# Kernel tuning notes

Hardware: AMD Instinct MI355X
Metric: run time of the kernel (lower is better)

Reference implementation:

```python
import jax, jax.numpy as jnp
import numpy as np
from jax import lax

K = 3          # kernel size
PAD = 1        # (K-1)//2
C = 64         # channels
RED = 16       # channel-attention reduction


def conv2d(x, w, b=None):
    # x [B,C,H,W], w [O,I,kh,kw]
    out = lax.conv_general_dilated(x, w, (1, 1), 'SAME',
                                   dimension_numbers=('NCHW', 'OIHW', 'NCHW'))
    if b is not None:
        out = out + b[None, :, None, None]
    return out


def rcab(x, w1, b1, w2, b2, caw1, cab1, caw2, cab2):
    res = conv2d(x, w1, b1)
    res = jax.nn.relu(res)
    res = conv2d(res, w2, b2)
    # channel attention: global avg pool -> 1x1 conv -> relu -> 1x1 conv -> sigmoid
    y = jnp.mean(res, axis=(2, 3), keepdims=True)
    y = jax.nn.relu(conv2d(y, caw1, cab1))
    y = jax.nn.sigmoid(conv2d(y, caw2, cab2))
    return res * y + x


def deform_conv(x, inter, fea, off_w, off_b, mask_w, mask_b, weight):
    # Modulated deformable conv: offsets/mask predicted from concat(inter, fea).
    B, Cc, H, W = x.shape
    KK = K * K
    guide = jnp.concatenate([inter, fea], axis=1)
    offset = conv2d(guide, off_w, off_b)                    # [B, 2*KK, H, W]
    mask = 2.0 * jax.nn.sigmoid(conv2d(guide, mask_w, mask_b))  # [B, KK, H, W]
    off = offset.reshape(B, KK, 2, H, W)
    oy, ox = off[:, :, 0], off[:, :, 1]                     # [B, KK, H, W]

    ky = (jnp.arange(KK) // K - PAD).astype(x.dtype)        # kernel tap y offsets
    kx = (jnp.arange(KK) % K - PAD).astype(x.dtype)
    ii = jnp.arange(H, dtype=x.dtype)[None, None, :, None]
    jj = jnp.arange(W, dtype=x.dtype)[None, None, None, :]
    ys = ii + ky[None, :, None, None] + oy                  # [B, KK, H, W]
    xs = jj + kx[None, :, None, None] + ox

    y0 = jnp.floor(ys); x0 = jnp.floor(xs)
    wy1 = ys - y0; wy0 = 1.0 - wy1
    wx1 = xs - x0; wx0 = 1.0 - wx1
    y0i = y0.astype(jnp.int32); x0i = x0.astype(jnp.int32)
    y1i = y0i + 1; x1i = x0i + 1

    x_flat = x.reshape(B, Cc, H * W)

    def gather(yi, xi):
        valid = ((yi >= 0) & (yi < H) & (xi >= 0) & (xi < W)).astype(x.dtype)
        idx = jnp.clip(yi, 0, H - 1) * W + jnp.clip(xi, 0, W - 1)   # [B,KK,H,W]
        idx = idx.reshape(B, KK * H * W)
        g = jax.vmap(lambda f, i: jnp.take(f, i, axis=1))(x_flat, idx)
        return g.reshape(B, Cc, KK, H, W) * valid[:, None]

    val = (gather(y0i, x0i) * (wy0 * wx0)[:, None]
           + gather(y0i, x1i) * (wy0 * wx1)[:, None]
           + gather(y1i, x0i) * (wy1 * wx0)[:, None]
           + gather(y1i, x1i) * (wy1 * wx1)[:, None])     # [B,C,KK,H,W]
    val = val * mask[:, None]
    w_flat = weight.reshape(weight.shape[0], Cc, KK)        # [O,I,KK]
    return jnp.einsum('bckhw,ock->bohw', val, w_flat)


def setup_inputs() -> dict:
    key = jax.random.key(0)
    ks = jax.random.split(key, 20)
    B, H, W = 4, 192, 192
    f32 = jnp.float32
    d = {
        'x':     jax.random.normal(ks[0], (B, C, H, W), f32),
        'inter': jax.random.normal(ks[1], (B, C, H, W), f32),
        'fea':   jax.random.normal(ks[2], (B, C, H, W), f32),
        # RCAB
        'rcab_w1': jax.random.normal(ks[3], (C, C, 3, 3), f32) * 0.05,
        'rcab_b1': jnp.zeros((C,), f32),
        'rcab_w2': jax.random.normal(ks[4], (C, C, 3, 3), f32) * 0.05,
        'rcab_b2': jnp.zeros((C,), f32),
        'ca_w1': jax.random.normal(ks[5], (C // RED, C, 1, 1), f32) * 0.05,
        'ca_b1': jnp.zeros((C // RED,), f32),
        'ca_w2': jax.random.normal(ks[6], (C, C // RED, 1, 1), f32) * 0.05,
        'ca_b2': jnp.zeros((C,), f32),
        # deformable conv offset/mask branch (input = concat(inter, fea) -> 2C)
        'off_w': jax.random.normal(ks[7], (2 * K * K, 2 * C, 3, 3), f32) * 0.01,
        'off_b': jnp.zeros((2 * K * K,), f32),
        'mask_w': jax.random.normal(ks[8], (K * K, 2 * C, 3, 3), f32) * 0.01,
        'mask_b': jnp.zeros((K * K,), f32),
        'deform_w': jax.random.normal(ks[9], (C, C, K, K), f32) * 0.05,
        # final conv
        'conv_w': jax.random.normal(ks[10], (C, C, 3, 3), f32) * 0.05,
        'conv_b': jnp.zeros((C,), f32),
    }
    return d


def reference(x, inter, fea, rcab_w1, rcab_b1, rcab_w2, rcab_b2,
              ca_w1, ca_b1, ca_w2, ca_b2,
              off_w, off_b, mask_w, mask_b, deform_w, conv_w, conv_b):
    out1 = rcab(x, rcab_w1, rcab_b1, rcab_w2, rcab_b2, ca_w1, ca_b1, ca_w2, ca_b2)
    out2 = deform_conv(out1, inter, fea, off_w, off_b, mask_w, mask_b, deform_w)
    return conv2d(out2 + out1, conv_w, conv_b)
```

## Files before the change

kernel.cpp:

```cpp
#include <hip/hip_runtime.h>
#include <hip/hip_bf16.h>
#include <hip/hip_fp16.h>
#include <math.h>

#define HSZ 192
#define WSZ 192
#define HWSZ (192*192)
#define PH 194
#define PP (PH*PH)
#define NB 4

typedef __attribute__((ext_vector_type(8))) short short8;
typedef __attribute__((ext_vector_type(4))) float f32x4;

__device__ inline unsigned short f2bf(float f) { __hip_bfloat16 h = __float2bfloat16(f); return *(unsigned short*)&h; }
__device__ inline float bf2f(__hip_bfloat16 h) { return __bfloat162float(h); }
__device__ inline float bflo(unsigned u) { return __uint_as_float(u << 16); }
__device__ inline float bfhi(unsigned u) { return __uint_as_float(u & 0xffff0000u); }

#define GLDS(SRC, DST) __builtin_amdgcn_global_load_lds( \
    (const __attribute__((address_space(1))) unsigned int*)(const void*)(SRC), \
    (__attribute__((address_space(3))) unsigned int*)(void*)(DST), 16, 0, 0)

#define MFMA(A,B,C) __builtin_amdgcn_mfma_f32_16x16x32_bf16((A),(B),(C),0,0,0)

__global__ void zb2_k(__hip_bfloat16* xn, __hip_bfloat16* r1, __hip_bfloat16* out1,
                      __hip_bfloat16* cat) {
  int job = blockIdx.y;
  __hip_bfloat16* buf = job == 0 ? xn : job == 1 ? r1 : job == 2 ? out1 : cat;
  int Cn = (job == 3) ? 128 : 64;
  int cg8 = Cn >> 3;
  int tot = NB * 772 * cg8;
  int idx = blockIdx.x * 256 + threadIdx.x;
  if (idx >= tot) return;
  int cg = idx % cg8; int rem = idx / cg8;
  int e = rem % 772; int b = rem / 772;
  int h, w2;
  if (e < 194) { h = 0; w2 = e; }
  else if (e < 388) { h = 193; w2 = e - 194; }
  else if (e < 580) { h = e - 388 + 1; w2 = 0; }
  else { h = e - 580 + 1; w2 = 193; }
  uint4 z = make_uint4(0, 0, 0, 0);
  *(uint4*)&buf[(((size_t)b * PH + h) * PH + w2) * Cn + cg * 8] = z;
}

__global__ void wts_k(const float* __restrict__ rw1, const float* __restrict__ rw2,
                      const float* __restrict__ cw, const float* __restrict__ offw,
                      const float* __restrict__ maskw, const float* __restrict__ offb,
                      const float* __restrict__ maskb, const float* __restrict__ dwv,
                      short* wt1, short* wt2c, short* wtf, short* wtom, float* ob,
                      short* wtb, float* meanz) {
  int job = blockIdx.y;
  int idx = blockIdx.x * 256 + threadIdx.x;
  if (job < 3) {
    const float* src = job == 0 ? rw1 : job == 1 ? rw2 : cw;
    short* dst = job == 0 ? wt1 : job == 1 ? wt2c : wtf;
    int kk = idx >> 12, rem = idx & 4095;
    int co = rem >> 6, ci = rem & 63;
    dst[idx] = (short)f2bf(src[(co * 64 + ci) * 9 + kk]);
  } else if (job == 3) {
    int kk = idx >> 12, rem = idx & 4095;
    int co = rem >> 7, ci = rem & 127;
    float v = 0.f;
    if (co < 18) v = offw[(co * 128 + ci) * 9 + kk];
    else if (co < 27) v = maskw[((co - 18) * 128 + ci) * 9 + kk];
    wtom[idx] = (short)f2bf(v);
    if (idx < 32) ob[idx] = idx < 18 ? offb[idx] : (idx < 27 ? maskb[idx - 18] : 0.f);
  } else {
    int o = idx / 576, rem = idx - o * 576;
    int kk = rem >> 6, ci = rem & 63;
    wtb[idx] = (short)f2bf(dwv[(o * 64 + ci) * 9 + kk]);
    if (blockIdx.x == 0 && threadIdx.x < 256) meanz[threadIdx.x] = 0.f;
  }
}

__global__ __launch_bounds__(256) void cvt_k(const float* __restrict__ x,
    const float* __restrict__ inter, const float* __restrict__ fea,
    __hip_bfloat16* __restrict__ xn, __hip_bfloat16* __restrict__ cat) {
  int job = blockIdx.z;
  const float* src = job == 0 ? x : job == 1 ? inter : fea;
  __hip_bfloat16* dst = job == 0 ? xn : cat;
  int Cdst = job == 0 ? 64 : 128;
  int coff = job == 2 ? 64 : 0;
  __shared__ float s[64][65];
  int p0 = blockIdx.x * 64; int b = blockIdx.y;
  int lane = threadIdx.x & 63, g = threadIdx.x >> 6;
#pragma unroll
  for (int i = 0; i < 16; ++i) {
    int c = i * 4 + g;
    s[c][lane] = src[((size_t)b * 64 + c) * HWSZ + p0 + lane];
  }
  __syncthreads();
  int pix = threadIdx.x >> 2, cg = threadIdx.x & 3;
  int h = p0 / WSZ, w0 = p0 - h * WSZ + pix;
  size_t addr = (((size_t)b * PH + h + 1) * PH + 1 + w0) * Cdst + coff + cg * 16;
  unsigned pk2[8];
#pragma unroll
  for (int t = 0; t < 8; ++t)
    pk2[t] = (unsigned)f2bf(s[cg * 16 + 2 * t][pix]) | ((unsigned)f2bf(s[cg * 16 + 2 * t + 1][pix]) << 16);
  *(uint4*)&dst[addr]     = make_uint4(pk2[0], pk2[1], pk2[2], pk2[3]);
  *(uint4*)&dst[addr + 8] = make_uint4(pk2[4], pk2[5], pk2[6], pk2[7]);
}

template<int OUT_MODE, bool RELU, bool MEANACC>
__global__ __launch_bounds__(256, 2) void conv_mfma_k(
    const __hip_bfloat16* __restrict__ inp, const short* __restrict__ wt,
    const float* __restrict__ bias, __hip_bfloat16* __restrict__ outB,
    float* __restrict__ outF, float* __restrict__ meanout) {
  int flat = (blockIdx.x & 7) * 96 + (blockIdx.x >> 3);
  const int b = flat / 192, h = flat - (flat / 192) * 192;
  const int tid = threadIdx.x, lane = tid & 63, wid = tid >> 6;
  const int q = lane >> 4, r16 = lane & 15;
  __shared__ __align__(16) short tile[3 * 200 * 64];
  __shared__ float smean[4][64];

  {
    const char* gb = (const char*)(inp + ((size_t)b * PH + h) * (PH * 64));
    for (int s = wid; s < 75; s += 4) {
      int rr = s / 25, si = s - rr * 25;
      int pix = 8 * si + (lane >> 3);
      const char* src = gb + (size_t)rr * (PH * 128) + pix * 128
                      + ((((lane & 7) ^ ((lane >> 3) & 7))) << 4);
      GLDS(src, tile + rr * 12800 + si * 512);
    }
  }

  f32x4 acc[3][4];
  if (OUT_MODE == 0) {
#pragma unroll
    for (int nf = 0; nf < 4; ++nf) {
      float4 bv = *(const float4*)&bias[nf * 16 + q * 4];
      f32x4 v; v[0] = bv.x; v[1] = bv.y; v[2] = bv.z; v[3] = bv.w;
      acc[0][nf] = v; acc[1][nf] = v; acc[2][nf] = v;
    }
  } else {
#pragma unroll
    for (int nf = 0; nf < 4; ++nf) {
      float bs = bias[nf * 16 + r16];
      f32x4 v; v[0] = bs; v[1] = bs; v[2] = bs; v[3] = bs;
      acc[0][nf] = v; acc[1][nf] = v; acc[2][nf] = v;
    }
  }
  __syncthreads();

  const int wm0 = wid * 48;
  for (int kk = 0; kk < 9; ++kk) {
    const int ky = kk / 3, kx = kk - ky * 3;
    short8 bfr[2][4];
    const short* wk = wt + kk * 4096 + r16 * 64 + q * 8;
#pragma unroll
    for (int nf = 0; nf < 4; ++nf) {
      bfr[0][nf] = *(const short8*)(wk + nf * 1024);
      bfr[1][nf] = *(const short8*)(wk + nf * 1024 + 32);
    }
#pragma unroll
    for (int mf = 0; mf < 3; ++mf) {
      int pix = wm0 + mf * 16 + r16 + kx;
      const char* ab = (const char*)tile + ky * 25600 + pix * 128;
      int sw = (pix & 7) << 4;
      short8 a0 = *(const short8*)(ab + ((q << 4) ^ sw));
      short8 a1 = *(const short8*)(ab + (((q + 4) << 4) ^ sw));
#pragma unroll
      for (int nf = 0; nf < 4; ++nf) {
        if (OUT_MODE == 0) {
          acc[mf][nf] = MFMA(bfr[0][nf], a0, acc[mf][nf]);
          acc[mf][nf] = MFMA(bfr[1][nf], a1, acc[mf][nf]);
        } else {
          acc[mf][nf] = MFMA(a0, bfr[0][nf], acc[mf][nf]);
          acc[mf][nf] = MFMA(a1, bfr[1][nf], acc[mf][nf]);
        }
      }
    }
  }

  if (MEANACC) {
    float t[4][4];
#pragma unroll
    for (int nf = 0; nf < 4; ++nf)
#pragma unroll
      for (int rg = 0; rg < 4; ++rg)
        t[nf][rg] = acc[0][nf][rg] + acc[1][nf][rg] + acc[2][nf][rg];
#pragma unroll
    for (int m = 1; m < 16; m <<= 1)
#pragma unroll
      for (int nf = 0; nf < 4; ++nf)
#pragma unroll
        for (int rg = 0; rg < 4; ++rg)
          t[nf][rg] += __shfl_xor(t[nf][rg], m);
    if (r16 == 0)
#pragma unroll
      for (int nf = 0; nf < 4; ++nf)
#pragma unroll
        for (int rg = 0; rg < 4; ++rg)
          smean[wid][nf * 16 + q * 4 + rg] = t[nf][rg];
    __syncthreads();
    if (tid < 64)
      atomicAdd(&meanout[b * 64 + tid],
                (smean[0][tid] + smean[1][tid] + smean[2][tid] + smean[3][tid]) * (1.f / 36864.f));
  }

  if (OUT_MODE == 0) {
    __syncthreads();
#pragma unroll
    for (int mf = 0; mf < 3; ++mf)
#pragma unroll
      for (int nf = 0; nf < 4; ++nf) {
        f32x4 v = acc[mf][nf];
        if (RELU) { v[0] = fmaxf(v[0], 0.f); v[1] = fmaxf(v[1], 0.f); v[2] = fmaxf(v[2], 0.f); v[3] = fmaxf(v[3], 0.f); }
        unsigned lo = (unsigned)f2bf(v[0]) | ((unsigned)f2bf(v[1]) << 16);
        unsigned hi = (unsigned)f2bf(v[2]) | ((unsigned)f2bf(v[3]) << 16);
        int pix = wm0 + mf * 16 + r16;
        int byteoff = (pix * 128 + nf * 32 + q * 8) ^ ((pix & 7) << 4);
        *(uint2*)((char*)tile + byteoff) = make_uint2(lo, hi);
      }
    __syncthreads();
    char* orow = (char*)outB + ((((size_t)b * PH + h + 1) * PH + 1) * 64) * 2;
    for (int s = wid; s < 24; s += 4) {
      int pix = 8 * s + (lane >> 3);
      int g16 = ((lane & 7) ^ (pix & 7)) << 4;
      uint4 d = *(const uint4*)((const char*)tile + pix * 128 + g16);
      *(uint4*)(orow + pix * 128 + ((lane & 7) << 4)) = d;
    }
  } else {
    float* ob2 = outF + (size_t)b * 64 * HWSZ + h * WSZ;
#pragma unroll
    for (int mf = 0; mf < 3; ++mf)
#pragma unroll
      for (int nf = 0; nf < 4; ++nf) {
        int pix0 = wm0 + mf * 16 + q * 4;
        int co = nf * 16 + r16;
        *(f32x4*)&ob2[(size_t)co * HWSZ + pix0] = acc[mf][nf];
      }
  }
}

__global__ __launch_bounds__(256, 3) void offmask_mfma_k(
    const __hip_bfloat16* __restrict__ cat, const short* __restrict__ wt2,
    const float* __restrict__ ob, float* __restrict__ om) {
  const int h = blockIdx.x, b = blockIdx.y;
  const int tid = threadIdx.x, lane = tid & 63, wid = tid >> 6;
  const int q = lane >> 4, r16 = lane & 15;
  __shared__ __align__(16) short tile[200 * 128];

  f32x4 acc[3][2];
#pragma unroll
  for (int nf = 0; nf < 2; ++nf) {
    float bs = ob[nf * 16 + r16];
    f32x4 v; v[0] = bs; v[1] = bs; v[2] = bs; v[3] = bs;
    acc[0][nf] = v; acc[1][nf] = v; acc[2][nf] = v;
  }
  const char* gb = (const char*)(cat + ((size_t)b * PH + h) * (PH * 128));
  const int wm0 = wid * 48;

  for (int r = 0; r < 3; ++r) {
    __syncthreads();
    for (int s = wid; s < 50; s += 4) {
      int pix = 4 * s + (lane >> 4);
      const char* src = gb + (size_t)r * (PH * 256) + pix * 256
                      + ((((lane & 15) ^ (pix & 15))) << 4);
      GLDS(src, tile + s * 512);
    }
    __syncthreads();
    for (int kx = 0; kx < 3; ++kx) {
      int kk = r * 3 + kx;
      short8 bfr[4][2];
      const short* wk = wt2 + kk * 4096 + r16 * 128 + q * 8;
#pragma unroll
      for (int c4 = 0; c4 < 4; ++c4) {
        bfr[c4][0] = *(const short8*)(wk + c4 * 32);
        bfr[c4][1] = *(const short8*)(wk + 2048 + c4 * 32);
      }
#pragma unroll
      for (int mf = 0; mf < 3; ++mf) {
        int pix = wm0 + mf * 16 + r16 + kx;
        const char* ab = (const char*)tile + pix * 256;
        int sw = (pix & 15) << 4;
        short8 a0 = *(const short8*)(ab + ((q << 4) ^ sw));
        short8 a1 = *(const short8*)(ab + (((4 + q) << 4) ^ sw));
        short8 a2 = *(const short8*)(ab + (((8 + q) << 4) ^ sw));
        short8 a3 = *(const short8*)(ab + (((12 + q) << 4) ^ sw));
        acc[mf][0] = MFMA(a0, bfr[0][0], acc[mf][0]); acc[mf][1] = MFMA(a0, bfr[0][1], acc[mf][1]);
        acc[mf][0] = MFMA(a1, bfr[1][0], acc[mf][0]); acc[mf][1] = MFMA(a1, bfr[1][1], acc[mf][1]);
        acc[mf][0] = MFMA(a2, bfr[2][0], acc[mf][0]); acc[mf][1] = MFMA(a2, bfr[2][1], acc[mf][1]);
        acc[mf][0] = MFMA(a3, bfr[3][0], acc[mf][0]); acc[mf][1] = MFMA(a3, bfr[3][1], acc[mf][1]);
      }
    }
  }
#pragma unroll
  for (int mf = 0; mf < 3; ++mf)
#pragma unroll
    for (int nf = 0; nf < 2; ++nf) {
      int co = nf * 16 + r16;
      if (co < 27) {
        f32x4 v = acc[mf][nf];
        if (co >= 18) {
          v[0] = 2.f / (1.f + expf(-v[0])); v[1] = 2.f / (1.f + expf(-v[1]));
          v[2] = 2.f / (1.f + expf(-v[2])); v[3] = 2.f / (1.f + expf(-v[3]));
        }
        *(f32x4*)&om[((size_t)(b * 27 + co)) * HWSZ + h * WSZ + wm0 + mf * 16 + q * 4] = v;
      }
    }
}

__global__ void ca_k(const float* __restrict__ mean, const float* __restrict__ w1, const float* __restrict__ b1,
                     const float* __restrict__ w2, const float* __restrict__ b2, float* __restrict__ y) {
  __shared__ float s_m[4][64];
  __shared__ float s_t[4][4];
  int tid = threadIdx.x;
  int b = tid >> 6, c = tid & 63;
  s_m[b][c] = mean[tid];
  __syncthreads();
  if (tid < 16) {
    int bb = tid >> 2, r = tid & 3;
    float s = b1[r];
    for (int cc = 0; cc < 64; ++cc) s += w1[r * 64 + cc] * s_m[bb][cc];
    s_t[bb][r] = fmaxf(s, 0.f);
  }
  __syncthreads();
  float v = b2[c];
  for (int r = 0; r < 4; ++r) v += w2[c * 4 + r] * s_t[b][r];
  y[tid] = 1.f / (1.f + expf(-v));
}

__global__ __launch_bounds__(256) void out1_k(const __hip_bfloat16* __restrict__ res, const __hip_bfloat16* __restrict__ xn,
    const float* __restrict__ y, __hip_bfloat16* __restrict__ out1) {
  int idx = blockIdx.x * 256 + threadIdx.x;
  int b = idx / 294912; int rem = idx - b * 294912;
  int p = rem >> 3, c8 = rem & 7;
  int hh = p / WSZ, ww = p - hh * WSZ;
  size_t off = ((size_t)b * PP + (size_t)(hh + 1) * PH + ww + 1) * 64 + c8 * 8;
  const __hip_bfloat16* rp = res + off;
  const __hip_bfloat16* xp = xn + off;
  __hip_bfloat16* op = out1 + off;
  const float* yb = y + b * 64 + c8 * 8;
  unsigned pk[4];
#pragma unroll
  for (int t = 0; t < 4; ++t) {
    float v0 = bf2f(rp[2 * t]) * yb[2 * t] + bf2f(xp[2 * t]);
    float v1 = bf2f(rp[2 * t + 1]) * yb[2 * t + 1] + bf2f(xp[2 * t + 1]);
    pk[t] = (unsigned)f2bf(v0) | ((unsigned)f2bf(v1) << 16);
  }
  *(uint4*)op = make_uint4(pk[0], pk[1], pk[2], pk[3]);
}

__global__ __launch_bounds__(256) void deform_mfma_k(
    const __hip_bfloat16* __restrict__ nhwc, const float* __restrict__ om,
    const short* __restrict__ wtb, __hip_bfloat16* __restrict__ fin) {
  int blk = (blockIdx.x & 7) * 576 + (blockIdx.x >> 3);
  int b = blk / 1152;
  int p0 = (blk - b * 1152) * 32;
  int tid = threadIdx.x, lane = tid & 63, wid = tid >> 6;
  int q = lane >> 4, r16 = lane & 15;
  __shared__ __align__(16) short sA[2][32][64];
  __shared__ __half2 s_bw[2][9][32];
  __shared__ int s_pk[9][32];

  const float* omb = om + (size_t)b * 27 * HWSZ + p0;
  for (int e = tid; e < 288; e += 256) {
    int kk = e >> 5, pix = e & 31;
    int p = p0 + pix;
    int h = p / WSZ, w2 = p - h * WSZ;
    float oy = omb[(size_t)(2 * kk) * HWSZ + pix];
    float ox = omb[(size_t)(2 * kk + 1) * HWSZ + pix];
    float m2 = omb[(size_t)(18 + kk) * HWSZ + pix];
    float ys = (float)(h + kk / 3 - 1) + oy;
    float xs = (float)(w2 + kk % 3 - 1) + ox;
    float y0f = floorf(ys), x0f = floorf(xs);
    float wy1 = ys - y0f, wx1 = xs - x0f;
    float wy0 = 1.f - wy1, wx0 = 1.f - wx1;
    int y0 = (int)y0f, x0i = (int)x0f;
    int y1 = y0 + 1, x1 = x0i + 1;
    float vy0 = (y0 >= 0 && y0 < HSZ) ? 1.f : 0.f;
    float vx0 = (x0i >= 0 && x0i < WSZ) ? 1.f : 0.f;
    float vy1 = (y1 >= 0 && y1 < HSZ) ? 1.f : 0.f;
    float vx1 = (x1 >= 0 && x1 < WSZ) ? 1.f : 0.f;
    int y0c = min(max(y0, 0), HSZ - 1), x0c = min(max(x0i, 0), WSZ - 1);
    int y1c = min(max(y1, 0), HSZ - 1), x1c = min(max(x1, 0), WSZ - 1);
    s_bw[0][kk][pix] = __floats2half2_rn(wy0 * wx0 * m2 * vy0 * vx0, wy0 * wx1 * m2 * vy0 * vx1);
    s_bw[1][kk][pix] = __floats2half2_rn(wy1 * wx0 * m2 * vy1 * vx0, wy1 * wx1 * m2 * vy1 * vx1);
    s_pk[kk][pix] = ((((y0c + 1) * PH) + x0c + 1) << 2) | ((y1c - y0c) << 1) | (x1c - x0c);
  }
  __syncthreads();

  const __hip_bfloat16* nb = nhwc + (size_t)b * PP * 64;
  const int spix = tid >> 3, lg = tid & 7;
  const int swz = (spix & 7) << 4;
  const int rsw = (r16 & 7) << 4;

  uint4 A0, B0, C0, D0, A1, B1, C1, D1, A2, B2, C2, D2;
  float2 wab0, wcd0, wab1, wcd1, wab2, wcd2;

#define ISSUE_R(KK, Av, Bv, Cv, Dv, Wab, Wcd) do { \
    Wab = __half22float2(s_bw[0][KK][spix]); \
    Wcd = __half22float2(s_bw[1][KK][spix]); \
    int pk_ = s_pk[KK][spix]; \
    int i00_ = pk_ >> 2, dy_ = (pk_ >> 1) & 1, dx_ = pk_ & 1; \
    const __hip_bfloat16* g_ = nb + (size_t)i00_ * 64 + lg * 8; \
    Av = *(const uint4*)g_; \
    Bv = *(const uint4*)(g_ + dx_ * 64); \
    Cv = *(const uint4*)(g_ + dy_ * (PH * 64)); \
    Dv = *(const uint4*)(g_ + (dy_ * PH + dx_) * 64); \
  } while (0)
#define CSTORE_R(BUFOFF, Av, Bv, Cv, Dv, Wab, Wcd) do { \
    const unsigned* ap_ = (const unsigned*)&Av; const unsigned* bp_ = (const unsigned*)&Bv; \
    const unsigned* cp_ = (const unsigned*)&Cv; const unsigned* dp_ = (const unsigned*)&Dv; \
    unsigned o_[4]; \
    _Pragma("unroll") \
    for (int j_ = 0; j_ < 4; ++j_) { \
      float lo_ = Wab.x * bflo(ap_[j_]) + Wab.y * bflo(bp_[j_]) + Wcd.x * bflo(cp_[j_]) + Wcd.y * bflo(dp_[j_]); \
      float hi_ = Wab.x * bfhi(ap_[j_]) + Wab.y * bfhi(bp_[j_]) + Wcd.x * bfhi(cp_[j_]) + Wcd.y * bfhi(dp_[j_]); \
      o_[j_] = (unsigned)f2bf(lo_) | ((unsigned)f2bf(hi_) << 16); \
    } \
    *(uint4*)((char*)sA + (BUFOFF) + spix * 128 + ((lg * 16) ^ swz)) = make_uint4(o_[0], o_[1], o_[2], o_[3]); \
  } while (0)

  ISSUE_R(0, A0, B0, C0, D0, wab0, wcd0);
  CSTORE_R(0, A0, B0, C0, D0, wab0, wcd0);
  ISSUE_R(1, A0, B0, C0, D0, wab0, wcd0);
  ISSUE_R(2, A1, B1, C1, D1, wab1, wcd1);
  ISSUE_R(3, A2, B2, C2, D2, wab2, wcd2);

  f32x4 acc0 = (f32x4){0.f, 0.f, 0.f, 0.f};
  f32x4 acc1 = (f32x4){0.f, 0.f, 0.f, 0.f};
  const short* wrow = wtb + (size_t)(wid * 16 + r16) * 576;
  const char* a0base = (const char*)sA + r16 * 128;
  const char* a1base = (const char*)sA + (r16 + 16) * 128;

#pragma unroll
  for (int kk = 0; kk < 9; ++kk) {
    const int bo = (kk & 1) * 4096;
    __syncthreads();
#pragma unroll
    for (int s = 0; s < 2; ++s) {
      short8 wf = *(const short8*)(wrow + kk * 64 + s * 32 + q * 8);
      int off = bo + ((s * 64 + q * 16) ^ rsw);
      short8 va = *(const short8*)(a0base + off);
      short8 vb = *(const short8*)(a1base + off);
      acc0 = MFMA(wf, va, acc0);
      acc1 = MFMA(wf, vb, acc1);
    }
    if (kk < 8) {
      const int nbo = ((kk + 1) & 1) * 4096;
      const int rs = kk % 3;
      if (rs == 0) {
        CSTORE_R(nbo, A0, B0, C0, D0, wab0, wcd0);
        if (kk + 4 <= 8) ISSUE_R(kk + 4, A0, B0, C0, D0, wab0, wcd0);
      } else if (rs == 1) {
        CSTORE_R(nbo, A1, B1, C1, D1, wab1, wcd1);
        if (kk + 4 <= 8) ISSUE_R(kk + 4, A1, B1, C1, D1, wab1, wcd1);
      } else {
        CSTORE_R(nbo, A2, B2, C2, D2, wab2, wcd2);
        if (kk + 4 <= 8) ISSUE_R(kk + 4, A2, B2, C2, D2, wab2, wcd2);
      }
    }
  }

  int h0 = p0 / WSZ, w0 = p0 - h0 * WSZ;
  size_t ro = ((size_t)(h0 + 1) * PH + w0 + 1) * 64;
  const __hip_bfloat16* resid = nb + ro;
  __hip_bfloat16* fp = fin + (size_t)b * PP * 64 + ro;
#pragma unroll
  for (int nf = 0; nf < 2; ++nf) {
    f32x4 av = nf ? acc1 : acc0;
    int pix = r16 + nf * 16;
    int co = wid * 16 + q * 4;
    const unsigned* rr = (const unsigned*)(resid + (size_t)pix * 64 + co);
    unsigned r0 = rr[0], r1 = rr[1];
    float o0 = av[0] + bflo(r0);
    float o1 = av[1] + bfhi(r0);
    float o2 = av[2] + bflo(r1);
    float o3 = av[3] + bfhi(r1);
    uint2 pk2 = make_uint2((unsigned)f2bf(o0) | ((unsigned)f2bf(o1) << 16),
                           (unsigned)f2bf(o2) | ((unsigned)f2bf(o3) << 16));
    *(uint2*)(fp + (size_t)pix * 64 + co) = pk2;
  }
#undef ISSUE_R
#undef CSTORE_R
}

extern "C" void kernel_launch(void* const* d_in, const int* in_sizes, int n_in,
                              void* d_out, int out_size, void* d_ws, size_t ws_size,
                              hipStream_t stream) {
  (void)in_sizes; (void)n_in; (void)out_size; (void)ws_size;
  const float* x     = (const float*)d_in[0];
  const float* inter = (const float*)d_in[1];
  const float* fea   = (const float*)d_in[2];
  const float* rw1   = (const float*)d_in[3];
  const float* rb1   = (const float*)d_in[4];
  const float* rw2   = (const float*)d_in[5];
  const float* rb2   = (const float*)d_in[6];
  const float* caw1  = (const float*)d_in[7];
  const float* cab1  = (const float*)d_in[8];
  const float* caw2  = (const float*)d_in[9];
  const float* cab2  = (const float*)d_in[10];
  const float* offw  = (const float*)d_in[11];
  const float* offb  = (const float*)d_in[12];
  const float* maskw = (const float*)d_in[13];
  const float* maskb = (const float*)d_in[14];
  const float* dw    = (const float*)d_in[15];
  const float* cw    = (const float*)d_in[16];
  const float* cb    = (const float*)d_in[17];

  char* w = (char*)d_ws;
  const size_t P64 = (size_t)NB * PP * 64 * 2 + 4096;
  const size_t PCAT = (size_t)NB * PP * 128 * 2 + 4096;
  __hip_bfloat16* xn   = (__hip_bfloat16*)(w);
  __hip_bfloat16* r1   = (__hip_bfloat16*)(w + P64);
  __hip_bfloat16* res  = (__hip_bfloat16*)(w + 2 * P64);
  __hip_bfloat16* out1 = (__hip_bfloat16*)(w + 3 * P64);
  __hip_bfloat16* cat  = (__hip_bfloat16*)(w + 4 * P64);
  char* tail = w + 4 * P64 + PCAT;
  short* wt1  = (short*)tail; tail += 73728;
  short* wt2c = (short*)tail; tail += 73728;
  short* wtf  = (short*)tail; tail += 73728;
  short* wtom = (short*)tail; tail += 73728;
  float* obb  = (float*)tail; tail += 128;
  short* wtb  = (short*)tail; tail += 73728;
  float* mean = (float*)tail; tail += 1024;
  float* yv   = (float*)tail; tail += 1024;
  float* omb  = (float*)res;
  __hip_bfloat16* fin = r1;

  zb2_k<<<dim3(194, 4), 256, 0, stream>>>(xn, r1, out1, cat);
  wts_k<<<dim3(144, 5), 256, 0, stream>>>(rw1, rw2, cw, offw, maskw, offb, maskb, dw,
                                          wt1, wt2c, wtf, wtom, obb, wtb, mean);
  cvt_k<<<dim3(576, 4, 3), 256, 0, stream>>>(x, inter, fea, xn, cat);

  conv_mfma_k<0, true , false><<<768, 256, 0, stream>>>(xn, wt1, rb1, r1, nullptr, nullptr);
  conv_mfma_k<0, false, true ><<<768, 256, 0, stream>>>(r1, wt2c, rb2, res, nullptr, mean);
  ca_k<<<1, 256, 0, stream>>>(mean, caw1, cab1, caw2, cab2, yv);
  out1_k<<<4608, 256, 0, stream>>>(res, xn, yv, out1);
  offmask_mfma_k<<<dim3(192, 4), 256, 0, stream>>>(cat, wtom, obb, omb);
  deform_mfma_k<<<NB * 1152, 256, 0, stream>>>(out1, omb, wtb, fin);
  conv_mfma_k<1, false, false><<<768, 256, 0, stream>>>(fin, wtf, cb, nullptr, (float*)d_out, nullptr);
}
```

Baseline: 267.1 us.

## Prefetch conv weights, fuse channel attention into out1, pack bf16 conversions

The conv and offset/mask MFMA kernels now double-buffer weight fragments in registers, loading the next tap's weights while the current tap's MFMAs run, and their tap loops are fully unrolled. The single-block channel-attention kernel is removed: each out1 block recomputes the small CA MLP with a wave reduction and computes sigmoids inline, saving one launch. The deform kernel's bilinear blend uses packed float2 math and v_cvt_pk_bf16_f32, and raises wave priority around its MFMA section. In exchange the kernels use more registers, and out1 redundantly recomputes the CA weights in every block.

```diff
diff --git a/kernel.cpp b/kernel.cpp
--- a/kernel.cpp
+++ b/kernel.cpp
@@ -12,11 +12,15 @@
 
 typedef __attribute__((ext_vector_type(8))) short short8;
 typedef __attribute__((ext_vector_type(4))) float f32x4;
+typedef __attribute__((ext_vector_type(2))) float f32x2;
 
 __device__ inline unsigned short f2bf(float f) { __hip_bfloat16 h = __float2bfloat16(f); return *(unsigned short*)&h; }
 __device__ inline float bf2f(__hip_bfloat16 h) { return __bfloat162float(h); }
 __device__ inline float bflo(unsigned u) { return __uint_as_float(u << 16); }
 __device__ inline float bfhi(unsigned u) { return __uint_as_float(u & 0xffff0000u); }
+__device__ inline f32x2 up2(unsigned u) {
+  f32x2 r; r[0] = __uint_as_float(u << 16); r[1] = __uint_as_float(u & 0xffff0000u); return r;
+}
 
 #define GLDS(SRC, DST) __builtin_amdgcn_global_load_lds( \
     (const __attribute__((address_space(1))) unsigned int*)(const void*)(SRC), \
@@ -141,17 +145,30 @@
       acc[0][nf] = v; acc[1][nf] = v; acc[2][nf] = v;
     }
   }
+
+  short8 bfr[2][2][4];
+  {
+    const short* wk0 = wt + r16 * 64 + q * 8;
+#pragma unroll
+    for (int nf = 0; nf < 4; ++nf) {
+      bfr[0][0][nf] = *(const short8*)(wk0 + nf * 1024);
+      bfr[0][1][nf] = *(const short8*)(wk0 + nf * 1024 + 32);
+    }
+  }
   __syncthreads();
 
   const int wm0 = wid * 48;
+#pragma unroll
   for (int kk = 0; kk < 9; ++kk) {
     const int ky = kk / 3, kx = kk - ky * 3;
-    short8 bfr[2][4];
-    const short* wk = wt + kk * 4096 + r16 * 64 + q * 8;
-#pragma unroll
-    for (int nf = 0; nf < 4; ++nf) {
-      bfr[0][nf] = *(const short8*)(wk + nf * 1024);
-      bfr[1][nf] = *(const short8*)(wk + nf * 1024 + 32);
+    const int cur = kk & 1;
+    if (kk < 8) {
+      const short* wk = wt + (kk + 1) * 4096 + r16 * 64 + q * 8;
+#pragma unroll
+      for (int nf = 0; nf < 4; ++nf) {
+        bfr[cur ^ 1][0][nf] = *(const short8*)(wk + nf * 1024);
+        bfr[cur ^ 1][1][nf] = *(const short8*)(wk + nf * 1024 + 32);
+      }
     }
 #pragma unroll
     for (int mf = 0; mf < 3; ++mf) {
@@ -163,11 +180,11 @@
 #pragma unroll
       for (int nf = 0; nf < 4; ++nf) {
         if (OUT_MODE == 0) {
-          acc[mf][nf] = MFMA(bfr[0][nf], a0, acc[mf][nf]);
-          acc[mf][nf] = MFMA(bfr[1][nf], a1, acc[mf][nf]);
+          acc[mf][nf] = MFMA(bfr[cur][0][nf], a0, acc[mf][nf]);
+          acc[mf][nf] = MFMA(bfr[cur][1][nf], a1, acc[mf][nf]);
         } else {
-          acc[mf][nf] = MFMA(a0, bfr[0][nf], acc[mf][nf]);
-          acc[mf][nf] = MFMA(a1, bfr[1][nf], acc[mf][nf]);
+          acc[mf][nf] = MFMA(a0, bfr[cur][0][nf], acc[mf][nf]);
+          acc[mf][nf] = MFMA(a1, bfr[cur][1][nf], acc[mf][nf]);
         }
       }
     }
@@ -252,6 +269,17 @@
   const char* gb = (const char*)(cat + ((size_t)b * PH + h) * (PH * 128));
   const int wm0 = wid * 48;
 
+  short8 bfr[2][4][2];
+  {
+    const short* wk0 = wt2 + r16 * 128 + q * 8;
+#pragma unroll
+    for (int c4 = 0; c4 < 4; ++c4) {
+      bfr[0][c4][0] = *(const short8*)(wk0 + c4 * 32);
+      bfr[0][c4][1] = *(const short8*)(wk0 + 2048 + c4 * 32);
+    }
+  }
+
+#pragma unroll
   for (int r = 0; r < 3; ++r) {
     __syncthreads();
     for (int s = wid; s < 50; s += 4) {
@@ -261,14 +289,17 @@
       GLDS(src, tile + s * 512);
     }
     __syncthreads();
+#pragma unroll
     for (int kx = 0; kx < 3; ++kx) {
-      int kk = r * 3 + kx;
-      short8 bfr[4][2];
-      const short* wk = wt2 + kk * 4096 + r16 * 128 + q * 8;
-#pragma unroll
-      for (int c4 = 0; c4 < 4; ++c4) {
-        bfr[c4][0] = *(const short8*)(wk + c4 * 32);
-        bfr[c4][1] = *(const short8*)(wk + 2048 + c4 * 32);
+      const int kk = r * 3 + kx;
+      const int cur = kk & 1;
+      if (kk < 8) {
+        const short* wk = wt2 + (kk + 1) * 4096 + r16 * 128 + q * 8;
+#pragma unroll
+        for (int c4 = 0; c4 < 4; ++c4) {
+          bfr[cur ^ 1][c4][0] = *(const short8*)(wk + c4 * 32);
+          bfr[cur ^ 1][c4][1] = *(const short8*)(wk + 2048 + c4 * 32);
+        }
       }
 #pragma unroll
       for (int mf = 0; mf < 3; ++mf) {
@@ -279,10 +310,10 @@
         short8 a1 = *(const short8*)(ab + (((4 + q) << 4) ^ sw));
         short8 a2 = *(const short8*)(ab + (((8 + q) << 4) ^ sw));
         short8 a3 = *(const short8*)(ab + (((12 + q) << 4) ^ sw));
-        acc[mf][0] = MFMA(a0, bfr[0][0], acc[mf][0]); acc[mf][1] = MFMA(a0, bfr[0][1], acc[mf][1]);
-        acc[mf][0] = MFMA(a1, bfr[1][0], acc[mf][0]); acc[mf][1] = MFMA(a1, bfr[1][1], acc[mf][1]);
-        acc[mf][0] = MFMA(a2, bfr[2][0], acc[mf][0]); acc[mf][1] = MFMA(a2, bfr[2][1], acc[mf][1]);
-        acc[mf][0] = MFMA(a3, bfr[3][0], acc[mf][0]); acc[mf][1] = MFMA(a3, bfr[3][1], acc[mf][1]);
+        acc[mf][0] = MFMA(a0, bfr[cur][0][0], acc[mf][0]); acc[mf][1] = MFMA(a0, bfr[cur][0][1], acc[mf][1]);
+        acc[mf][0] = MFMA(a1, bfr[cur][1][0], acc[mf][0]); acc[mf][1] = MFMA(a1, bfr[cur][1][1], acc[mf][1]);
+        acc[mf][0] = MFMA(a2, bfr[cur][2][0], acc[mf][0]); acc[mf][1] = MFMA(a2, bfr[cur][2][1], acc[mf][1]);
+        acc[mf][0] = MFMA(a3, bfr[cur][3][0], acc[mf][0]); acc[mf][1] = MFMA(a3, bfr[cur][3][1], acc[mf][1]);
       }
     }
   }
@@ -302,43 +333,46 @@
     }
 }
 
-__global__ void ca_k(const float* __restrict__ mean, const float* __restrict__ w1, const float* __restrict__ b1,
-                     const float* __restrict__ w2, const float* __restrict__ b2, float* __restrict__ y) {
-  __shared__ float s_m[4][64];
-  __shared__ float s_t[4][4];
-  int tid = threadIdx.x;
-  int b = tid >> 6, c = tid & 63;
-  s_m[b][c] = mean[tid];
-  __syncthreads();
-  if (tid < 16) {
-    int bb = tid >> 2, r = tid & 3;
-    float s = b1[r];
-    for (int cc = 0; cc < 64; ++cc) s += w1[r * 64 + cc] * s_m[bb][cc];
-    s_t[bb][r] = fmaxf(s, 0.f);
-  }
-  __syncthreads();
-  float v = b2[c];
-  for (int r = 0; r < 4; ++r) v += w2[c * 4 + r] * s_t[b][r];
-  y[tid] = 1.f / (1.f + expf(-v));
-}
-
 __global__ __launch_bounds__(256) void out1_k(const __hip_bfloat16* __restrict__ res, const __hip_bfloat16* __restrict__ xn,
-    const float* __restrict__ y, __hip_bfloat16* __restrict__ out1) {
+    const float* __restrict__ mean, const float* __restrict__ w1, const float* __restrict__ b1,
+    const float* __restrict__ w2, const float* __restrict__ b2,
+    __hip_bfloat16* __restrict__ out1) {
   int idx = blockIdx.x * 256 + threadIdx.x;
   int b = idx / 294912; int rem = idx - b * 294912;
   int p = rem >> 3, c8 = rem & 7;
+  int lane = threadIdx.x & 63, wid = threadIdx.x >> 6;
+
+  __shared__ float s_t[4];
+  {
+    float prod = w1[wid * 64 + lane] * mean[b * 64 + lane];
+#pragma unroll
+    for (int m = 1; m < 64; m <<= 1) prod += __shfl_xor(prod, m);
+    if (lane == 0) s_t[wid] = fmaxf(prod + b1[wid], 0.f);
+  }
+  __syncthreads();
+  float t0 = s_t[0], t1 = s_t[1], t2 = s_t[2], t3 = s_t[3];
+
   int hh = p / WSZ, ww = p - hh * WSZ;
   size_t off = ((size_t)b * PP + (size_t)(hh + 1) * PH + ww + 1) * 64 + c8 * 8;
   const __hip_bfloat16* rp = res + off;
   const __hip_bfloat16* xp = xn + off;
   __hip_bfloat16* op = out1 + off;
-  const float* yb = y + b * 64 + c8 * 8;
   unsigned pk[4];
 #pragma unroll
   for (int t = 0; t < 4; ++t) {
-    float v0 = bf2f(rp[2 * t]) * yb[2 * t] + bf2f(xp[2 * t]);
-    float v1 = bf2f(rp[2 * t + 1]) * yb[2 * t + 1] + bf2f(xp[2 * t + 1]);
-    pk[t] = (unsigned)f2bf(v0) | ((unsigned)f2bf(v1) << 16);
+    float y0, y1;
+    {
+      int c = c8 * 8 + 2 * t;
+      const float4 wv0 = *(const float4*)&w2[c * 4];
+      const float4 wv1 = *(const float4*)&w2[(c + 1) * 4];
+      float v0 = b2[c]     + wv0.x * t0 + wv0.y * t1 + wv0.z * t2 + wv0.w * t3;
+      float v1 = b2[c + 1] + wv1.x * t0 + wv1.y * t1 + wv1.z * t2 + wv1.w * t3;
+      y0 = 1.f / (1.f + expf(-v0));
+      y1 = 1.f / (1.f + expf(-v1));
+    }
+    float o0 = bf2f(rp[2 * t]) * y0 + bf2f(xp[2 * t]);
+    float o1 = bf2f(rp[2 * t + 1]) * y1 + bf2f(xp[2 * t + 1]);
+    pk[t] = (unsigned)f2bf(o0) | ((unsigned)f2bf(o1) << 16);
   }
   *(uint4*)op = make_uint4(pk[0], pk[1], pk[2], pk[3]);
 }
@@ -407,9 +441,8 @@
     unsigned o_[4]; \
     _Pragma("unroll") \
     for (int j_ = 0; j_ < 4; ++j_) { \
-      float lo_ = Wab.x * bflo(ap_[j_]) + Wab.y * bflo(bp_[j_]) + Wcd.x * bflo(cp_[j_]) + Wcd.y * bflo(dp_[j_]); \
-      float hi_ = Wab.x * bfhi(ap_[j_]) + Wab.y * bfhi(bp_[j_]) + Wcd.x * bfhi(cp_[j_]) + Wcd.y * bfhi(dp_[j_]); \
-      o_[j_] = (unsigned)f2bf(lo_) | ((unsigned)f2bf(hi_) << 16); \
+      f32x2 v_ = up2(ap_[j_]) * Wab.x + up2(bp_[j_]) * Wab.y + up2(cp_[j_]) * Wcd.x + up2(dp_[j_]) * Wcd.y; \
+      asm("v_cvt_pk_bf16_f32 %0, %1, %2" : "=v"(o_[j_]) : "v"(v_[0]), "v"(v_[1])); \
     } \
     *(uint4*)((char*)sA + (BUFOFF) + spix * 128 + ((lg * 16) ^ swz)) = make_uint4(o_[0], o_[1], o_[2], o_[3]); \
   } while (0)
@@ -430,6 +463,7 @@
   for (int kk = 0; kk < 9; ++kk) {
     const int bo = (kk & 1) * 4096;
     __syncthreads();
+    __builtin_amdgcn_s_setprio(1);
 #pragma unroll
     for (int s = 0; s < 2; ++s) {
       short8 wf = *(const short8*)(wrow + kk * 64 + s * 32 + q * 8);
@@ -439,6 +473,7 @@
       acc0 = MFMA(wf, va, acc0);
       acc1 = MFMA(wf, vb, acc1);
     }
+    __builtin_amdgcn_s_setprio(0);
     if (kk < 8) {
       const int nbo = ((kk + 1) & 1) * 4096;
       const int rs = kk % 3;
@@ -517,7 +552,6 @@
   float* obb  = (float*)tail; tail += 128;
   short* wtb  = (short*)tail; tail += 73728;
   float* mean = (float*)tail; tail += 1024;
-  float* yv   = (float*)tail; tail += 1024;
   float* omb  = (float*)res;
   __hip_bfloat16* fin = r1;
 
@@ -528,8 +562,7 @@
 
   conv_mfma_k<0, true , false><<<768, 256, 0, stream>>>(xn, wt1, rb1, r1, nullptr, nullptr);
   conv_mfma_k<0, false, true ><<<768, 256, 0, stream>>>(r1, wt2c, rb2, res, nullptr, mean);
-  ca_k<<<1, 256, 0, stream>>>(mean, caw1, cab1, caw2, cab2, yv);
-  out1_k<<<4608, 256, 0, stream>>>(res, xn, yv, out1);
+  out1_k<<<4608, 256, 0, stream>>>(res, xn, mean, caw1, cab1, caw2, cab2, out1);
   offmask_mfma_k<<<dim3(192, 4), 256, 0, stream>>>(cat, wtom, obb, omb);
   deform_mfma_k<<<NB * 1152, 256, 0, stream>>>(out1, omb, wtb, fin);
   conv_mfma_k<1, false, false><<<768, 256, 0, stream>>>(fin, wtf, cb, nullptr, (float*)d_out, nullptr);
```

New measurement: 272.5 us. 1.02x slower.
